# Performance work log

Hardware: AMD Instinct MI355X
Metric: run time of the kernel (lower is better)

Reference implementation:

```python
import jax, jax.numpy as jnp
import numpy as np

N_NODES = 100000
N_EDGES = 1600000
D_IN = 64
D_OUT = 64


def setup_inputs() -> dict:
    key = jax.random.key(0)
    k1, k2, k3, k4, k5, k6 = jax.random.split(key, 6)
    x = jax.random.normal(k1, (N_NODES, D_IN), dtype=jnp.float32)
    weight = jax.random.normal(k2, (D_IN, D_OUT), dtype=jnp.float32) * (1.0 / np.sqrt(D_OUT))
    bias = jax.random.normal(k3, (D_OUT,), dtype=jnp.float32) * (1.0 / np.sqrt(D_OUT))
    adj_vals = jax.random.uniform(k4, (N_EDGES,), dtype=jnp.float32)
    src = jax.random.randint(k5, (N_EDGES,), 0, N_NODES, dtype=jnp.int32)
    dst = jax.random.randint(k6, (N_EDGES,), 0, N_NODES, dtype=jnp.int32)
    return {"x": x, "weight": weight, "bias": bias, "adj_vals": adj_vals, "src": src, "dst": dst}


def reference(x, weight, bias, adj_vals, src, dst):
    # support = X @ W  -> [N, D_OUT]
    support = jnp.dot(x, weight)
    # sparse adjacency matmul: out[dst] += adj_vals * support[src]
    msgs = adj_vals[:, None] * support[src]  # [E, D_OUT]
    out = jax.ops.segment_sum(msgs, dst, num_segments=N_NODES)
    return out + bias
```

## Files before the change

kernel.cpp:

```cpp
#include <hip/hip_runtime.h>

#define N_NODES 100000
#define N_EDGES 1600000
#define D 64

#define BN 64
#define NBUCK ((N_NODES + BN - 1) / BN)
#define CHW 256
#define CH ((N_EDGES + CHW - 1) / CHW)
#define CITER 13
#define CAP 2048
#define SMAX 2048
#define PAD 16
#define OVFMAX 32768
#define GEMM_THREADS (N_NODES * 16 / 2)
#define GEMM_BLKS ((GEMM_THREADS + 511) / 512)

static __device__ __forceinline__ unsigned short f2bf(float f) {
    unsigned u = __float_as_uint(f);
    u += 0x7FFFu + ((u >> 16) & 1u);
    return (unsigned short)(u >> 16);
}
static __device__ __forceinline__ float bf2f(unsigned short h) {
    return __uint_as_float((unsigned)h << 16);
}

__global__ __launch_bounds__(512) void gcn_main(const float* __restrict__ x,
                                                const float* __restrict__ w,
                                                unsigned short* __restrict__ support,
                                                const int* __restrict__ src,
                                                const int* __restrict__ dst,
                                                const float* __restrict__ adj,
                                                int* __restrict__ gcur,
                                                int* __restrict__ ovfcnt,
                                                int4* __restrict__ ovflist,
                                                int2* __restrict__ coarse) {
    __shared__ __align__(16) char smem[16384];
    int tid = threadIdx.x;

    if (blockIdx.x < CHW) {
        int* h = (int*)smem;
        int* cur = h + NBUCK;
        int wb = blockIdx.x;
        for (int i = tid; i < NBUCK; i += 512) h[i] = 0;
        __syncthreads();

        int e0 = wb * CH, e1 = min(e0 + CH, N_EDGES);
        int dreg[CITER], sreg[CITER];
        float areg[CITER];
        #pragma unroll
        for (int it = 0; it < CITER; ++it) {
            int e = e0 + tid + it * 512;
            dreg[it] = -1;
            if (e < e1) {
                dreg[it] = __builtin_nontemporal_load(&dst[e]);
                sreg[it] = __builtin_nontemporal_load(&src[e]);
                areg[it] = __builtin_nontemporal_load(&adj[e]);
                atomicAdd(&h[dreg[it] >> 6], 1);
            }
        }
        __syncthreads();

        for (int c = tid; c < NBUCK; c += 512) {
            int hc = h[c];
            if (hc) cur[c] = atomicAdd(&gcur[c * PAD], hc);
        }
        __syncthreads();

        #pragma unroll
        for (int it = 0; it < CITER; ++it) {
            if (dreg[it] >= 0) {
                int c = dreg[it] >> 6;
                int pos = atomicAdd(&cur[c], 1);
                if (pos < CAP) {
                    coarse[c * CAP + pos] =
                        make_int2(sreg[it] | ((dreg[it] & 63) << 17),
                                  __float_as_int(areg[it]));
                } else {
                    int op = atomicAdd(ovfcnt, 1);
                    if (op < OVFMAX)
                        ovflist[op] = make_int4(sreg[it], dreg[it],
                                                __float_as_int(areg[it]), 0);
                }
            }
        }
    } else {
        float4* wsh = (float4*)smem;
        const float4* w4 = (const float4*)w;
        for (int i = tid; i < 64 * 16; i += 512) wsh[i] = w4[i];
        __syncthreads();

        int idx = (blockIdx.x - CHW) * 512 + tid;
        if (idx < GEMM_THREADS) {
            int rowpair = idx >> 4;
            int c4 = idx & 15;
            long r0 = (long)rowpair * 2;
            const float4* xr0 = (const float4*)(x + r0 * D);
            const float4* xr1 = (const float4*)(x + (r0 + 1) * D);

            float4 a0 = make_float4(0.f, 0.f, 0.f, 0.f);
            float4 a1 = make_float4(0.f, 0.f, 0.f, 0.f);
            #pragma unroll 4
            for (int k4 = 0; k4 < 16; ++k4) {
                float4 xv0 = xr0[k4];
                float4 xv1 = xr1[k4];
                float4 w0 = wsh[(4 * k4 + 0) * 16 + c4];
                float4 w1 = wsh[(4 * k4 + 1) * 16 + c4];
                float4 w2 = wsh[(4 * k4 + 2) * 16 + c4];
                float4 w3 = wsh[(4 * k4 + 3) * 16 + c4];
                a0 += w0 * xv0.x + w1 * xv0.y + w2 * xv0.z + w3 * xv0.w;
                a1 += w0 * xv1.x + w1 * xv1.y + w2 * xv1.z + w3 * xv1.w;
            }
            ushort4* s4 = (ushort4*)support;
            s4[r0 * 16 + c4] = make_ushort4(f2bf(a0.x), f2bf(a0.y), f2bf(a0.z), f2bf(a0.w));
            s4[(r0 + 1) * 16 + c4] = make_ushort4(f2bf(a1.x), f2bf(a1.y), f2bf(a1.z), f2bf(a1.w));
        }
    }
}

__global__ __launch_bounds__(256) void gcn_bgather(const unsigned short* __restrict__ support,
                                                   const int2* __restrict__ coarse,
                                                   const int* __restrict__ gcur,
                                                   const float* __restrict__ bias,
                                                   float* __restrict__ out) {
    __shared__ int2 sE[SMAX];
    __shared__ int cntS[BN], loffS[BN], curS[BN];

    int tid = threadIdx.x, wv = tid >> 6, lane = tid & 63;
    int b = blockIdx.x;
    int tot = min(gcur[b * PAD], CAP);
    const int2* ce = coarse + (long)b * CAP;

    if (tid < BN) cntS[tid] = 0;
    __syncthreads();

    for (int e = tid; e < tot; e += 256)
        atomicAdd(&cntS[(ce[e].x >> 17) & 63], 1);
    __syncthreads();

    if (tid < BN) loffS[tid] = cntS[tid];
    __syncthreads();
    for (int off = 1; off < BN; off <<= 1) {
        int t = 0;
        if (tid < BN && tid >= off) t = loffS[tid - off];
        __syncthreads();
        if (tid < BN && tid >= off) loffS[tid] += t;
        __syncthreads();
    }
    if (tid < BN) {
        int excl = loffS[tid] - cntS[tid];
        loffS[tid] = excl;
        curS[tid] = excl;
    }
    __syncthreads();

    for (int e = tid; e < tot; e += 256) {
        int2 ed = ce[e];
        int nl = (ed.x >> 17) & 63;
        int pos = atomicAdd(&curS[nl], 1);
        sE[pos] = ed;
    }
    __syncthreads();

    int eg = lane >> 4;
    int L  = lane & 15;
    const uint2* sup2 = (const uint2*)support;
    const float4* bias4 = (const float4*)bias;
    float4* out4 = (float4*)out;
    float4 bv = bias4[L];

    for (int nl = wv * 16; nl < wv * 16 + 16; ++nl) {
        int start = loffS[nl];
        int avail = cntS[nl];
        float4 acc = make_float4(0.f, 0.f, 0.f, 0.f);
        for (int j = 0; j < avail; j += 16) {
            #pragma unroll
            for (int q = 0; q < 4; ++q) {
                int ei = j + q * 4 + eg;
                int2 ed = sE[start + min(ei, avail - 1)];
                float wgt = (ei < avail) ? __int_as_float(ed.y) : 0.f;
                uint2 p = sup2[(long)(ed.x & 0x1FFFF) * 16 + L];
                acc.x += wgt * __uint_as_float(p.x << 16);
                acc.y += wgt * __uint_as_float(p.x & 0xFFFF0000u);
                acc.z += wgt * __uint_as_float(p.y << 16);
                acc.w += wgt * __uint_as_float(p.y & 0xFFFF0000u);
            }
        }
        acc.x += __shfl_xor(acc.x, 16, 64); acc.y += __shfl_xor(acc.y, 16, 64);
        acc.z += __shfl_xor(acc.z, 16, 64); acc.w += __shfl_xor(acc.w, 16, 64);
        acc.x += __shfl_xor(acc.x, 32, 64); acc.y += __shfl_xor(acc.y, 32, 64);
        acc.z += __shfl_xor(acc.z, 32, 64); acc.w += __shfl_xor(acc.w, 32, 64);
        int n = b * BN + nl;
        if (lane < 16 && n < N_NODES) {
            float4 r = make_float4(acc.x + bv.x, acc.y + bv.y,
                                   acc.z + bv.z, acc.w + bv.w);
            out4[(long)n * 16 + L] = r;
        }
    }
}

__global__ __launch_bounds__(256) void gcn_ovffix(const int* __restrict__ ovfcnt,
                                                  const int4* __restrict__ ovflist,
                                                  const unsigned short* __restrict__ support,
                                                  float* __restrict__ out) {
    int n = *ovfcnt;
    if (n > OVFMAX) n = OVFMAX;
    int lane = threadIdx.x & 63, g = threadIdx.x >> 6;
    for (int i = g; i < n; i += 4) {
        int4 ed = ovflist[i];
        float v = __int_as_float(ed.z) * bf2f(support[(long)ed.x * D + lane]);
        atomicAdd(&out[(long)ed.y * D + lane], v);
    }
}

extern "C" void kernel_launch(void* const* d_in, const int* in_sizes, int n_in,
                              void* d_out, int out_size, void* d_ws, size_t ws_size,
                              hipStream_t stream) {
    const float* x      = (const float*)d_in[0];
    const float* weight = (const float*)d_in[1];
    const float* bias   = (const float*)d_in[2];
    const float* adj    = (const float*)d_in[3];
    const int*   src    = (const int*)d_in[4];
    const int*   dst    = (const int*)d_in[5];
    float* out = (float*)d_out;

    unsigned short* support = (unsigned short*)d_ws;
    int2* coarse = (int2*)(support + (long)N_NODES * D);
    int*  gcur   = (int*)(coarse + (long)NBUCK * CAP);
    int*  ovfcnt = gcur + NBUCK * PAD;
    int4* ovflist = (int4*)(ovfcnt + 4);

    hipMemsetAsync(gcur, 0, NBUCK * PAD * sizeof(int) + 16, stream);
    hipLaunchKernelGGL(gcn_main, dim3(CHW + GEMM_BLKS), dim3(512), 0, stream,
                       x, weight, support, src, dst, adj, gcur, ovfcnt, ovflist, coarse);
    hipLaunchKernelGGL(gcn_bgather, dim3(NBUCK), dim3(256), 0, stream,
                       support, coarse, gcur, bias, out);
    hipLaunchKernelGGL(gcn_ovffix, dim3(1), dim3(256), 0, stream,
                       ovfcnt, ovflist, support, out);
}
```

Before: 173.8 us.

## Interleave binning and GEMM blocks, reload edges, fold overflow fix into gather

Binning blocks are spread among the GEMM blocks (every seventh block id) so the atomic-heavy binning work overlaps with the GEMM instead of running as a separate leading group. Edge data is read twice from global memory instead of being held in registers, which lowers register pressure at the cost of extra loads. The separate single-block overflow kernel is removed: each gather block scans the overflow list for its own bucket, saving a launch but making every block read the overflow count and list. The gather inner loop is also unrolled by two.

```diff
diff --git a/kernel.cpp b/kernel.cpp
--- a/kernel.cpp
+++ b/kernel.cpp
@@ -8,13 +8,12 @@
 #define NBUCK ((N_NODES + BN - 1) / BN)
 #define CHW 256
 #define CH ((N_EDGES + CHW - 1) / CHW)
-#define CITER 13
 #define CAP 2048
 #define SMAX 2048
 #define PAD 16
 #define OVFMAX 32768
 #define GEMM_THREADS (N_NODES * 16 / 2)
-#define GEMM_BLKS ((GEMM_THREADS + 511) / 512)
+#define NBLK (CHW + 1563)
 
 static __device__ __forceinline__ unsigned short f2bf(float f) {
     unsigned u = __float_as_uint(f);
@@ -37,28 +36,19 @@
                                                 int2* __restrict__ coarse) {
     __shared__ __align__(16) char smem[16384];
     int tid = threadIdx.x;
-
-    if (blockIdx.x < CHW) {
+    int bid = blockIdx.x;
+    bool isbin = ((bid % 7) == 0) && ((bid / 7) < CHW);
+
+    if (isbin) {
         int* h = (int*)smem;
         int* cur = h + NBUCK;
-        int wb = blockIdx.x;
+        int wb = bid / 7;
         for (int i = tid; i < NBUCK; i += 512) h[i] = 0;
         __syncthreads();
 
         int e0 = wb * CH, e1 = min(e0 + CH, N_EDGES);
-        int dreg[CITER], sreg[CITER];
-        float areg[CITER];
-        #pragma unroll
-        for (int it = 0; it < CITER; ++it) {
-            int e = e0 + tid + it * 512;
-            dreg[it] = -1;
-            if (e < e1) {
-                dreg[it] = __builtin_nontemporal_load(&dst[e]);
-                sreg[it] = __builtin_nontemporal_load(&src[e]);
-                areg[it] = __builtin_nontemporal_load(&adj[e]);
-                atomicAdd(&h[dreg[it] >> 6], 1);
-            }
-        }
+        for (int e = e0 + tid; e < e1; e += 512)
+            atomicAdd(&h[dst[e] >> 6], 1);
         __syncthreads();
 
         for (int c = tid; c < NBUCK; c += 512) {
@@ -67,21 +57,19 @@
         }
         __syncthreads();
 
-        #pragma unroll
-        for (int it = 0; it < CITER; ++it) {
-            if (dreg[it] >= 0) {
-                int c = dreg[it] >> 6;
-                int pos = atomicAdd(&cur[c], 1);
-                if (pos < CAP) {
-                    coarse[c * CAP + pos] =
-                        make_int2(sreg[it] | ((dreg[it] & 63) << 17),
-                                  __float_as_int(areg[it]));
-                } else {
-                    int op = atomicAdd(ovfcnt, 1);
-                    if (op < OVFMAX)
-                        ovflist[op] = make_int4(sreg[it], dreg[it],
-                                                __float_as_int(areg[it]), 0);
-                }
+        for (int e = e0 + tid; e < e1; e += 512) {
+            int d = dst[e];
+            int s = src[e];
+            float a = adj[e];
+            int c = d >> 6;
+            int pos = atomicAdd(&cur[c], 1);
+            if (pos < CAP) {
+                coarse[c * CAP + pos] =
+                    make_int2(s | ((d & 63) << 17), __float_as_int(a));
+            } else {
+                int op = atomicAdd(ovfcnt, 1);
+                if (op < OVFMAX)
+                    ovflist[op] = make_int4(s, d, __float_as_int(a), 0);
             }
         }
     } else {
@@ -90,7 +78,9 @@
         for (int i = tid; i < 64 * 16; i += 512) wsh[i] = w4[i];
         __syncthreads();
 
-        int idx = (blockIdx.x - CHW) * 512 + tid;
+        int bins_before = min(bid / 7 + 1, CHW);
+        int gb = bid - bins_before;
+        int idx = gb * 512 + tid;
         if (idx < GEMM_THREADS) {
             int rowpair = idx >> 4;
             int c4 = idx & 15;
@@ -121,6 +111,8 @@
 __global__ __launch_bounds__(256) void gcn_bgather(const unsigned short* __restrict__ support,
                                                    const int2* __restrict__ coarse,
                                                    const int* __restrict__ gcur,
+                                                   const int* __restrict__ ovfcnt,
+                                                   const int4* __restrict__ ovflist,
                                                    const float* __restrict__ bias,
                                                    float* __restrict__ out) {
     __shared__ int2 sE[SMAX];
@@ -173,6 +165,7 @@
         int start = loffS[nl];
         int avail = cntS[nl];
         float4 acc = make_float4(0.f, 0.f, 0.f, 0.f);
+        #pragma unroll 2
         for (int j = 0; j < avail; j += 16) {
             #pragma unroll
             for (int q = 0; q < 4; ++q) {
@@ -197,19 +190,15 @@
             out4[(long)n * 16 + L] = r;
         }
     }
-}
-
-__global__ __launch_bounds__(256) void gcn_ovffix(const int* __restrict__ ovfcnt,
-                                                  const int4* __restrict__ ovflist,
-                                                  const unsigned short* __restrict__ support,
-                                                  float* __restrict__ out) {
-    int n = *ovfcnt;
-    if (n > OVFMAX) n = OVFMAX;
-    int lane = threadIdx.x & 63, g = threadIdx.x >> 6;
-    for (int i = g; i < n; i += 4) {
+
+    __syncthreads();
+    int no = min(*ovfcnt, OVFMAX);
+    for (int i = wv; i < no; i += 4) {
         int4 ed = ovflist[i];
-        float v = __int_as_float(ed.z) * bf2f(support[(long)ed.x * D + lane]);
-        atomicAdd(&out[(long)ed.y * D + lane], v);
+        if ((ed.y >> 6) == b) {
+            float v = __int_as_float(ed.z) * bf2f(support[(long)ed.x * D + lane]);
+            atomicAdd(&out[(long)ed.y * D + lane], v);
+        }
     }
 }
 
@@ -231,10 +220,8 @@
     int4* ovflist = (int4*)(ovfcnt + 4);
 
     hipMemsetAsync(gcur, 0, NBUCK * PAD * sizeof(int) + 16, stream);
-    hipLaunchKernelGGL(gcn_main, dim3(CHW + GEMM_BLKS), dim3(512), 0, stream,
+    hipLaunchKernelGGL(gcn_main, dim3(NBLK), dim3(512), 0, stream,
                        x, weight, support, src, dst, adj, gcur, ovfcnt, ovflist, coarse);
     hipLaunchKernelGGL(gcn_bgather, dim3(NBUCK), dim3(256), 0, stream,
-                       support, coarse, gcur, bias, out);
-    hipLaunchKernelGGL(gcn_ovffix, dim3(1), dim3(256), 0, stream,
-                       ovfcnt, ovflist, support, out);
-}
+                       support, coarse, gcur, ovfcnt, ovflist, bias, out);
+}
```

Measured after the change: 192.9 us. 11.0% more time.
